# Kernel optimization log

Measured on AMD Instinct MI355X. Metric: run time of the kernel, lower is better.

## Reference

```python
import jax, jax.numpy as jnp
import numpy as np

B, C, H, W = 8, 512, 32, 32
MID = 64  # in_ch // k = 512 // 8
BN_EPS = 1e-5


def conv1x1(x, Wt, b):
    # x: [B,C,H,W], Wt: [O,C], b: [O]
    return jnp.einsum('bchw,oc->bohw', x, Wt) + b[None, :, None, None]


def batchnorm(x, gamma, beta):
    # train-mode BN: batch statistics over (B,H,W)
    mu = jnp.mean(x, axis=(0, 2, 3), keepdims=True)
    var = jnp.var(x, axis=(0, 2, 3), keepdims=True)
    xn = (x - mu) * jax.lax.rsqrt(var + BN_EPS)
    return xn * gamma[None, :, None, None] + beta[None, :, None, None]


def setup_inputs() -> dict:
    key = jax.random.key(0)
    ks = jax.random.split(key, 8)
    scale = 1.0 / np.sqrt(C)
    x = jax.random.normal(ks[0], (B, C, H, W), dtype=jnp.float32)
    Wf = jax.random.normal(ks[1], (MID, C), dtype=jnp.float32) * scale
    Wg = jax.random.normal(ks[2], (MID, C), dtype=jnp.float32) * scale
    Wh = jax.random.normal(ks[3], (MID, C), dtype=jnp.float32) * scale
    Wv = jax.random.normal(ks[4], (C, MID), dtype=jnp.float32) * (1.0 / np.sqrt(MID))
    return {
        'x': x,
        'Wf': Wf, 'bf': jnp.zeros((MID,), jnp.float32),
        'gamma_f': jnp.ones((MID,), jnp.float32), 'beta_f': jnp.zeros((MID,), jnp.float32),
        'Wg': Wg, 'bg': jnp.zeros((MID,), jnp.float32),
        'gamma_g': jnp.ones((MID,), jnp.float32), 'beta_g': jnp.zeros((MID,), jnp.float32),
        'Wh': Wh, 'bh': jnp.zeros((MID,), jnp.float32),
        'Wv': Wv, 'bv': jnp.zeros((C,), jnp.float32),
    }


def reference(x, Wf, bf, gamma_f, beta_f, Wg, bg, gamma_g, beta_g, Wh, bh, Wv, bv):
    b, c, h, w = x.shape
    hw = h * w
    f_x = jax.nn.relu(batchnorm(conv1x1(x, Wf, bf), gamma_f, beta_f)).reshape(b, MID, hw)
    g_x = jax.nn.relu(batchnorm(conv1x1(x, Wg, bg), gamma_g, beta_g)).reshape(b, MID, hw)
    h_x = conv1x1(x, Wh, bh).reshape(b, MID, hw)
    # z = f_x^T @ g_x : [B, HW, HW]
    z = jnp.einsum('bcn,bcm->bnm', f_x, g_x)
    # spectral normalization by the top singular value
    S = jnp.linalg.svd(z, compute_uv=False)  # sorted descending
    sigma = S[:, 0][:, None, None]
    attn = z / sigma
    # attn @ h_x^T -> [B, HW, MID], then permute to [B, MID, H, W]
    z2 = jnp.einsum('bnm,bcm->bcn', attn, h_x).reshape(b, MID, h, w)
    return conv1x1(z2, Wv, bv) + x
```

## Files before the change

kernel.cpp:

```cpp
#include <hip/hip_runtime.h>

#define B_   8
#define C_   512
#define HW_  1024
#define MID_ 64
#define NCOL (B_*HW_)
#define NROWS 192
#define EPS  1e-5f

#define YOFF  0
#define YSZ   (NROWS*NCOL)
#define SSOFF (YOFF+YSZ)
#define SSSZ  256
#define WOFF  (SSOFF+SSSZ)
#define WSZ   98304
#define CPOFF (WOFF+WSZ)

typedef unsigned short u16;
typedef __attribute__((ext_vector_type(8))) short short8;
typedef __attribute__((ext_vector_type(4))) float f32x4;

__device__ __forceinline__ u16 f2bf(float f) {
  unsigned u = __float_as_uint(f);
  unsigned r = u + 0x7fffu + ((u >> 16) & 1u);
  return (u16)(r >> 16);
}
__device__ __forceinline__ float bf2f(u16 h) {
  return __uint_as_float(((unsigned)h) << 16);
}
#define MFMA_B16(a,b,c) __builtin_amdgcn_mfma_f32_16x16x32_bf16(a,b,c,0,0,0)

__global__ __launch_bounds__(256) void k_prep(
    const float* __restrict__ Wf, const float* __restrict__ Wg,
    const float* __restrict__ Wh, float* __restrict__ ws)
{
  u16* Whi = (u16*)(ws + WOFF);
  u16* Wlo = Whi + NROWS*C_;
  const int e4 = blockIdx.x*256 + threadIdx.x;
  const int e  = e4*4;
  const int row = e >> 9, k = e & 511;
  const float* src = (row < 64) ? &Wf[row*C_ + k]
                   : (row < 128) ? &Wg[(row-64)*C_ + k]
                   : &Wh[(row-128)*C_ + k];
  const float4 v = *reinterpret_cast<const float4*>(src);
  u16 h0=f2bf(v.x), h1=f2bf(v.y), h2=f2bf(v.z), h3=f2bf(v.w);
  u16 l0=f2bf(v.x-bf2f(h0)), l1=f2bf(v.y-bf2f(h1)), l2=f2bf(v.z-bf2f(h2)), l3=f2bf(v.w-bf2f(h3));
  uint2 ph; ph.x = (unsigned)h0 | ((unsigned)h1<<16); ph.y = (unsigned)h2 | ((unsigned)h3<<16);
  uint2 pl; pl.x = (unsigned)l0 | ((unsigned)l1<<16); pl.y = (unsigned)l2 | ((unsigned)l3<<16);
  *reinterpret_cast<uint2*>(&Whi[e]) = ph;
  *reinterpret_cast<uint2*>(&Wlo[e]) = pl;
}

__global__ __launch_bounds__(256) void k_conv(
    const float* __restrict__ x,
    const float* __restrict__ bf, const float* __restrict__ bg, const float* __restrict__ bh,
    float* __restrict__ ws)
{
  __shared__ u16 Xh[8*32*8];
  __shared__ u16 Xl[8*32*8];
  const u16* Whi = (const u16*)(ws + WOFF);
  const u16* Wlo = Whi + NROWS*C_;
  const int n0  = blockIdx.x * 32;
  const int b   = n0 >> 10;
  const int hw0 = n0 & 1023;
  const int t   = threadIdx.x;
  const int lane = t & 63;
  const int wid  = t >> 6;
  const int wrow0 = wid * 48;
  const int cst  = t & 31;
  const int kg2  = t >> 5;
  const int lm   = lane & 15;
  const int lk   = lane >> 4;

  f32x4 acc[3][2];
  #pragma unroll
  for (int i=0;i<3;++i) { acc[i][0]=(f32x4)0.f; acc[i][1]=(f32x4)0.f; }

  for (int kk = 0; kk < C_; kk += 64) {
    __syncthreads();
    {
      const float* xp = x + ((size_t)(b*C_ + kk + kg2*8))*HW_ + hw0 + cst;
      u16 hb[8], lb[8];
      #pragma unroll
      for (int i=0;i<8;++i) {
        const float v = xp[(size_t)i*HW_];
        hb[i] = f2bf(v); lb[i] = f2bf(v - bf2f(hb[i]));
      }
      uint4 ph, pl;
      ph.x=(unsigned)hb[0]|((unsigned)hb[1]<<16); ph.y=(unsigned)hb[2]|((unsigned)hb[3]<<16);
      ph.z=(unsigned)hb[4]|((unsigned)hb[5]<<16); ph.w=(unsigned)hb[6]|((unsigned)hb[7]<<16);
      pl.x=(unsigned)lb[0]|((unsigned)lb[1]<<16); pl.y=(unsigned)lb[2]|((unsigned)lb[3]<<16);
      pl.z=(unsigned)lb[4]|((unsigned)lb[5]<<16); pl.w=(unsigned)lb[6]|((unsigned)lb[7]<<16);
      *reinterpret_cast<uint4*>(&Xh[(kg2*32+cst)*8]) = ph;
      *reinterpret_cast<uint4*>(&Xl[(kg2*32+cst)*8]) = pl;
    }
    __syncthreads();
    #pragma unroll
    for (int kb = 0; kb < 2; ++kb) {
      short8 bhf[2], blf[2];
      #pragma unroll
      for (int nt = 0; nt < 2; ++nt) {
        const int col = nt*16 + lm;
        const int idx = ((kb*4 + lk)*32 + col)*8;
        bhf[nt] = *reinterpret_cast<const short8*>(&Xh[idx]);
        blf[nt] = *reinterpret_cast<const short8*>(&Xl[idx]);
      }
      #pragma unroll
      for (int mt = 0; mt < 3; ++mt) {
        const int row = wrow0 + mt*16 + lm;
        const size_t widx = (size_t)row*C_ + kk + kb*32 + lk*8;
        const short8 ah = *reinterpret_cast<const short8*>(&Whi[widx]);
        const short8 al = *reinterpret_cast<const short8*>(&Wlo[widx]);
        #pragma unroll
        for (int nt = 0; nt < 2; ++nt) {
          acc[mt][nt] = MFMA_B16(ah, bhf[nt], acc[mt][nt]);
          acc[mt][nt] = MFMA_B16(al, bhf[nt], acc[mt][nt]);
          acc[mt][nt] = MFMA_B16(ah, blf[nt], acc[mt][nt]);
        }
      }
    }
  }
  #pragma unroll
  for (int mt = 0; mt < 3; ++mt) {
    const int rbase = wrow0 + mt*16;
    const float* bp = (rbase < 64) ? bf : (rbase < 128) ? bg : bh;
    const int rloc0 = (rbase & 63) + lk*4;
    #pragma unroll
    for (int nt = 0; nt < 2; ++nt) {
      const int col = n0 + nt*16 + lm;
      #pragma unroll
      for (int r = 0; r < 4; ++r) {
        const int row = rbase + lk*4 + r;
        ws[YOFF + (size_t)row*NCOL + col] = acc[mt][nt][r] + bp[rloc0 + r];
      }
    }
  }
}

__global__ __launch_bounds__(256) void k_stats(
    const float* __restrict__ gamma_f, const float* __restrict__ beta_f,
    const float* __restrict__ gamma_g, const float* __restrict__ beta_g,
    float* __restrict__ ws)
{
  const int r = blockIdx.x;
  const float4* Yr = reinterpret_cast<const float4*>(ws + YOFF + (size_t)r*NCOL);
  const int t = threadIdx.x;
  float s = 0.f, s2 = 0.f;
  for (int n = t; n < NCOL/4; n += 256) {
    const float4 v = Yr[n];
    s  += (v.x+v.y)+(v.z+v.w);
    s2 += (v.x*v.x+v.y*v.y)+(v.z*v.z+v.w*v.w);
  }
  __shared__ float sh[256], sh2[256];
  sh[t] = s; sh2[t] = s2;
  __syncthreads();
  for (int st = 128; st > 0; st >>= 1) {
    if (t < st) { sh[t] += sh[t+st]; sh2[t] += sh2[t+st]; }
    __syncthreads();
  }
  if (t == 0) {
    const float mean = sh[0] * (1.0f/NCOL);
    const float var  = sh2[0] * (1.0f/NCOL) - mean*mean;
    float g, be; int j;
    if (r < 64) { j = r;     g = gamma_f[j]; be = beta_f[j]; }
    else        { j = r-64;  g = gamma_g[j]; be = beta_g[j]; }
    const float sc = g * rsqrtf(var + EPS);
    const float sf = be - mean*sc;
    if (r < 64) { ws[SSOFF + j]       = sc; ws[SSOFF + 64  + j] = sf; }
    else        { ws[SSOFF + 128 + j] = sc; ws[SSOFF + 192 + j] = sf; }
  }
}

__global__ __launch_bounds__(256) void k_cpart(float* __restrict__ ws, int nchunk)
{
  __shared__ u16 Sh[3][64][72];
  __shared__ u16 Sl[3][64][72];
  const int chunk = blockIdx.x, b = blockIdx.y;
  const int chunkcols = 1024 / nchunk;
  const int bcol0 = b*1024 + chunk*chunkcols;
  const float* Y = ws + YOFF;
  const float* SS = ws + SSOFF;
  const int t = threadIdx.x;
  const int lane = t & 63, wid = t >> 6;
  const int lm = lane & 15, lk = lane >> 4;
  const int mt0 = (wid >> 1) * 2;
  const int nt0 = (wid & 1) * 2;

  f32x4 acc[3][2][2];
  #pragma unroll
  for (int p=0;p<3;++p) for (int i=0;i<2;++i) for (int j=0;j<2;++j) acc[p][i][j]=(f32x4)0.f;

  for (int kk = 0; kk < chunkcols; kk += 64) {
    __syncthreads();
    for (int q = t; q < 3072; q += 256) {
      const int mm = q >> 10, rem = q & 1023;
      const int r = rem >> 4, c4 = (rem & 15) * 4;
      const float4 v = *reinterpret_cast<const float4*>(
          &Y[(size_t)(mm*64 + r)*NCOL + bcol0 + kk + c4]);
      float v0, v1, v2, v3;
      if (mm < 2) {
        const float sc = SS[mm*128 + r], sf = SS[mm*128 + 64 + r];
        v0 = fmaxf(sc*v.x+sf, 0.f); v1 = fmaxf(sc*v.y+sf, 0.f);
        v2 = fmaxf(sc*v.z+sf, 0.f); v3 = fmaxf(sc*v.w+sf, 0.f);
      } else { v0=v.x; v1=v.y; v2=v.z; v3=v.w; }
      const u16 h0=f2bf(v0), h1=f2bf(v1), h2=f2bf(v2), h3=f2bf(v3);
      uint2 ph; ph.x=(unsigned)h0|((unsigned)h1<<16); ph.y=(unsigned)h2|((unsigned)h3<<16);
      uint2 pl;
      pl.x=(unsigned)f2bf(v0-bf2f(h0)) | ((unsigned)f2bf(v1-bf2f(h1))<<16);
      pl.y=(unsigned)f2bf(v2-bf2f(h2)) | ((unsigned)f2bf(v3-bf2f(h3))<<16);
      *reinterpret_cast<uint2*>(&Sh[mm][r][c4]) = ph;
      *reinterpret_cast<uint2*>(&Sl[mm][r][c4]) = pl;
    }
    __syncthreads();
    #pragma unroll
    for (int kb = 0; kb < 2; ++kb) {
      const int ko = kb*32 + lk*8;
      short8 ah[3][2], al[3][2];
      #pragma unroll
      for (int m = 0; m < 3; ++m)
        #pragma unroll
        for (int mi = 0; mi < 2; ++mi) {
          const int row = (mt0+mi)*16 + lm;
          ah[m][mi] = *reinterpret_cast<const short8*>(&Sh[m][row][ko]);
          al[m][mi] = *reinterpret_cast<const short8*>(&Sl[m][row][ko]);
        }
      short8 bhf[2][2], blf[2][2];
      #pragma unroll
      for (int m = 0; m < 2; ++m)
        #pragma unroll
        for (int ni = 0; ni < 2; ++ni) {
          const int row = (nt0+ni)*16 + lm;
          bhf[m][ni] = *reinterpret_cast<const short8*>(&Sh[m][row][ko]);
          blf[m][ni] = *reinterpret_cast<const short8*>(&Sl[m][row][ko]);
        }
      #pragma unroll
      for (int p = 0; p < 3; ++p) {
        const int am = p;
        const int bm = (p==0) ? 0 : 1;
        #pragma unroll
        for (int mi = 0; mi < 2; ++mi)
          #pragma unroll
          for (int ni = 0; ni < 2; ++ni) {
            acc[p][mi][ni] = MFMA_B16(ah[am][mi], bhf[bm][ni], acc[p][mi][ni]);
            acc[p][mi][ni] = MFMA_B16(al[am][mi], bhf[bm][ni], acc[p][mi][ni]);
            acc[p][mi][ni] = MFMA_B16(ah[am][mi], blf[bm][ni], acc[p][mi][ni]);
          }
      }
    }
  }
  float* cp = ws + CPOFF;
  #pragma unroll
  for (int p = 0; p < 3; ++p) {
    float* base = cp + ((size_t)((b*3+p)*nchunk + chunk))*4096;
    #pragma unroll
    for (int mi = 0; mi < 2; ++mi)
      #pragma unroll
      for (int ni = 0; ni < 2; ++ni) {
        const int col = (nt0+ni)*16 + lm;
        #pragma unroll
        for (int r = 0; r < 4; ++r) {
          const int row = (mt0+mi)*16 + lk*4 + r;
          base[(size_t)row*64 + col] = acc[p][mi][ni][r];
        }
      }
  }
}

__global__ __launch_bounds__(256) void k_creduce(float* __restrict__ ws, int nchunk)
{
  const int m = blockIdx.y;
  const int q = blockIdx.x*256 + threadIdx.x;
  const float4* src = reinterpret_cast<const float4*>(ws + CPOFF) + (size_t)m*nchunk*1024;
  const size_t cmoff = (size_t)CPOFF + (size_t)B_*3*nchunk*4096;
  float4 s = {0.f,0.f,0.f,0.f};
  for (int ch = 0; ch < nchunk; ++ch) {
    const float4 p = src[(size_t)ch*1024 + q];
    s.x+=p.x; s.y+=p.y; s.z+=p.z; s.w+=p.w;
  }
  *(reinterpret_cast<float4*>(ws + cmoff) + (size_t)m*1024 + q) = s;
}

__global__ __launch_bounds__(64) void k_sigma(float* __restrict__ ws, int nchunk)
{
  const int b = blockIdx.x;
  const int lane = threadIdx.x;
  const size_t cmoff = (size_t)CPOFF + (size_t)B_*3*nchunk*4096;
  const size_t isoff = cmoff + 24*4096;
  const float* Cf = ws + cmoff + (size_t)(b*3+0)*4096;
  const float* Cg = ws + cmoff + (size_t)(b*3+1)*4096;
  __shared__ float vsh[64];
  __shared__ float ush[64];
  float cfr[64], cgr[64];
  #pragma unroll
  for (int k4 = 0; k4 < 16; ++k4) {
    const float4 fa = *reinterpret_cast<const float4*>(&Cf[lane*64 + k4*4]);
    const float4 fc = *reinterpret_cast<const float4*>(&Cg[lane*64 + k4*4]);
    cfr[k4*4+0]=fa.x; cfr[k4*4+1]=fa.y; cfr[k4*4+2]=fa.z; cfr[k4*4+3]=fa.w;
    cgr[k4*4+0]=fc.x; cgr[k4*4+1]=fc.y; cgr[k4*4+2]=fc.z; cgr[k4*4+3]=fc.w;
  }
  float vloc = 0.125f;
  vsh[lane] = vloc;
  __syncthreads();
  float lambda = 0.f;
  #define NIT 20
  for (int it = 0; it <= NIT; ++it) {
    float u0=0.f,u1=0.f,u2=0.f,u3=0.f;
    #pragma unroll
    for (int j4 = 0; j4 < 16; ++j4) {
      const float4 vq = *reinterpret_cast<const float4*>(&vsh[j4*4]);
      u0 += cfr[j4*4+0]*vq.x; u1 += cfr[j4*4+1]*vq.y;
      u2 += cfr[j4*4+2]*vq.z; u3 += cfr[j4*4+3]*vq.w;
    }
    ush[lane] = (u0+u1)+(u2+u3);
    __syncthreads();
    float w0=0.f,w1=0.f,w2=0.f,w3=0.f;
    #pragma unroll
    for (int j4 = 0; j4 < 16; ++j4) {
      const float4 uq = *reinterpret_cast<const float4*>(&ush[j4*4]);
      w0 += cgr[j4*4+0]*uq.x; w1 += cgr[j4*4+1]*uq.y;
      w2 += cgr[j4*4+2]*uq.z; w3 += cgr[j4*4+3]*uq.w;
    }
    const float w = (w0+w1)+(w2+w3);
    if (it == NIT) {
      float num = vloc * w;
      #pragma unroll
      for (int off = 32; off > 0; off >>= 1) num += __shfl_xor(num, off);
      lambda = num;
    } else {
      float n2 = w*w;
      #pragma unroll
      for (int off = 32; off > 0; off >>= 1) n2 += __shfl_xor(n2, off);
      const float rn = rsqrtf(fmaxf(n2, 1e-30f));
      vloc = w * rn;
      vsh[lane] = vloc;
      __syncthreads();
    }
  }
  if (lane == 0) ws[isoff + b] = rsqrtf(fmaxf(lambda, 1e-30f));
}

__global__ __launch_bounds__(256) void k_ufold(const float* __restrict__ Wv,
                                               float* __restrict__ ws, int nchunk)
{
  __shared__ float Wt[64][64];
  __shared__ float Tl[64][64];
  const int rt = blockIdx.x, b = blockIdx.y;
  const size_t cmoff = (size_t)CPOFF + (size_t)B_*3*nchunk*4096;
  const size_t isoff = cmoff + 24*4096;
  const size_t uoff  = isoff + 16;
  const float* T = ws + cmoff + (size_t)(b*3+2)*4096;
  const float isig = ws[isoff + b];
  const int t = threadIdx.x;
  const int ti = t >> 4, tj = t & 15;
  for (int q = t; q < 1024; q += 256)
    *(reinterpret_cast<float4*>(&Tl[0][0]) + q) = *(reinterpret_cast<const float4*>(T) + q);
  for (int q = t; q < 1024; q += 256) {
    const int row = q >> 4;
    const int c4  = (q & 15) * 4;
    const float4 wv = *reinterpret_cast<const float4*>(&Wv[(size_t)(rt*64+row)*64 + c4]);
    Wt[c4+0][row]=wv.x; Wt[c4+1][row]=wv.y; Wt[c4+2][row]=wv.z; Wt[c4+3][row]=wv.w;
  }
  __syncthreads();
  float acc[4][4] = {};
  #pragma unroll
  for (int c = 0; c < 64; ++c) {
    const float4 a  = *reinterpret_cast<const float4*>(&Wt[c][ti*4]);
    const float4 bb = *reinterpret_cast<const float4*>(&Tl[c][tj*4]);
    acc[0][0]+=a.x*bb.x; acc[0][1]+=a.x*bb.y; acc[0][2]+=a.x*bb.z; acc[0][3]+=a.x*bb.w;
    acc[1][0]+=a.y*bb.x; acc[1][1]+=a.y*bb.y; acc[1][2]+=a.y*bb.z; acc[1][3]+=a.y*bb.w;
    acc[2][0]+=a.z*bb.x; acc[2][1]+=a.z*bb.y; acc[2][2]+=a.z*bb.z; acc[2][3]+=a.z*bb.w;
    acc[3][0]+=a.w*bb.x; acc[3][1]+=a.w*bb.y; acc[3][2]+=a.w*bb.z; acc[3][3]+=a.w*bb.w;
  }
  #pragma unroll
  for (int i = 0; i < 4; ++i) {
    float4 o; o.x = acc[i][0]*isig; o.y = acc[i][1]*isig; o.z = acc[i][2]*isig; o.w = acc[i][3]*isig;
    *reinterpret_cast<float4*>(&ws[uoff + ((size_t)b*512 + rt*64 + ti*4+i)*64 + tj*4]) = o;
  }
}

__global__ __launch_bounds__(256) void k_final(
    const float* __restrict__ x, const float* __restrict__ bv,
    float* __restrict__ out, const float* __restrict__ ws, int nchunk)
{
  __shared__ float Ut[64][64];
  __shared__ float Fl[64][64];
  const int nt = blockIdx.x, ot = blockIdx.y, b = blockIdx.z;
  const size_t uoff = (size_t)CPOFF + (size_t)B_*3*nchunk*4096 + 24*4096 + 16;
  const float* scF = ws + SSOFF; const float* sfF = ws + SSOFF + 64;
  const int t = threadIdx.x;
  const int ti = t >> 4, tj = t & 15;
  for (int q = t; q < 1024; q += 256) {
    const int row = q >> 4;
    const int k4  = (q & 15) * 4;
    const float4 uv = *reinterpret_cast<const float4*>(
        &ws[uoff + ((size_t)b*512 + ot*64 + row)*64 + k4]);
    Ut[k4+0][row]=uv.x; Ut[k4+1][row]=uv.y; Ut[k4+2][row]=uv.z; Ut[k4+3][row]=uv.w;
  }
  for (int q = t; q < 1024; q += 256) {
    const int k  = q >> 4;
    const int c4 = (q & 15) * 4;
    const float4 yv = *reinterpret_cast<const float4*>(
        &ws[YOFF + (size_t)k*NCOL + b*1024 + nt*64 + c4]);
    const float s = scF[k], f = sfF[k];
    Fl[k][c4+0]=fmaxf(s*yv.x+f,0.f); Fl[k][c4+1]=fmaxf(s*yv.y+f,0.f);
    Fl[k][c4+2]=fmaxf(s*yv.z+f,0.f); Fl[k][c4+3]=fmaxf(s*yv.w+f,0.f);
  }
  __syncthreads();
  float acc[4][4] = {};
  #pragma unroll
  for (int k = 0; k < 64; ++k) {
    const float4 a  = *reinterpret_cast<const float4*>(&Ut[k][ti*4]);
    const float4 bb = *reinterpret_cast<const float4*>(&Fl[k][tj*4]);
    acc[0][0]+=a.x*bb.x; acc[0][1]+=a.x*bb.y; acc[0][2]+=a.x*bb.z; acc[0][3]+=a.x*bb.w;
    acc[1][0]+=a.y*bb.x; acc[1][1]+=a.y*bb.y; acc[1][2]+=a.y*bb.z; acc[1][3]+=a.y*bb.w;
    acc[2][0]+=a.z*bb.x; acc[2][1]+=a.z*bb.y; acc[2][2]+=a.z*bb.z; acc[2][3]+=a.z*bb.w;
    acc[3][0]+=a.w*bb.x; acc[3][1]+=a.w*bb.y; acc[3][2]+=a.w*bb.z; acc[3][3]+=a.w*bb.w;
  }
  #pragma unroll
  for (int i = 0; i < 4; ++i) {
    const int oc = ot*64 + ti*4 + i;
    const float bvv = bv[oc];
    const size_t base = ((size_t)b*C_ + oc)*HW_ + nt*64 + tj*4;
    const float4 xv = *reinterpret_cast<const float4*>(&x[base]);
    float4 o;
    o.x = acc[i][0]+bvv+xv.x; o.y = acc[i][1]+bvv+xv.y;
    o.z = acc[i][2]+bvv+xv.z; o.w = acc[i][3]+bvv+xv.w;
    *reinterpret_cast<float4*>(&out[base]) = o;
  }
}

extern "C" void kernel_launch(void* const* d_in, const int* in_sizes, int n_in,
                              void* d_out, int out_size, void* d_ws, size_t ws_size,
                              hipStream_t stream) {
  (void)in_sizes; (void)n_in; (void)out_size;
  const float* x       = (const float*)d_in[0];
  const float* Wf      = (const float*)d_in[1];
  const float* bf      = (const float*)d_in[2];
  const float* gamma_f = (const float*)d_in[3];
  const float* beta_f  = (const float*)d_in[4];
  const float* Wg      = (const float*)d_in[5];
  const float* bg      = (const float*)d_in[6];
  const float* gamma_g = (const float*)d_in[7];
  const float* beta_g  = (const float*)d_in[8];
  const float* Wh      = (const float*)d_in[9];
  const float* bh      = (const float*)d_in[10];
  const float* Wv      = (const float*)d_in[11];
  const float* bv      = (const float*)d_in[12];
  float* out = (float*)d_out;
  float* ws  = (float*)d_ws;

  auto need = [](int nc) -> size_t {
    return ((size_t)CPOFF + (size_t)B_*3*nc*4096 + 24*4096 + 16 + (size_t)B_*512*64) * 4;
  };
  const int nchunk = (ws_size >= need(16)) ? 16 : (ws_size >= need(8)) ? 8 : 4;

  k_prep   <<<96,             256, 0, stream>>>(Wf, Wg, Wh, ws);
  k_conv   <<<256,            256, 0, stream>>>(x, bf, bg, bh, ws);
  k_stats  <<<128,            256, 0, stream>>>(gamma_f, beta_f, gamma_g, beta_g, ws);
  k_cpart  <<<dim3(nchunk,8), 256, 0, stream>>>(ws, nchunk);
  k_creduce<<<dim3(4,24),     256, 0, stream>>>(ws, nchunk);
  k_sigma  <<<8,               64, 0, stream>>>(ws, nchunk);
  k_ufold  <<<dim3(8,8),      256, 0, stream>>>(Wv, ws, nchunk);
  k_final  <<<dim3(16,8,8),   256, 0, stream>>>(x, bv, out, ws, nchunk);
}
```

Measured before the change: 92.85 us.

## Fuse all stages into one persistent kernel with atomic grid barriers

Replaces the eight separate kernel launches with a single persistent 256-block kernel that runs each stage in turn and separates them with a software grid barrier built on an atomic counter. Shared memory is overlaid through a union, and the work split is changed per stage (stats split across two blocks per row, cpart with 32 fixed chunks, final handling four column tiles per block). This removes launch overhead and inter-kernel gaps between many small stages. In exchange it relies on all 256 blocks being co-resident for the spin barrier, and each barrier adds its own latency.

```diff
diff --git a/kernel.cpp b/kernel.cpp
--- a/kernel.cpp
+++ b/kernel.cpp
@@ -3,18 +3,26 @@
 #define B_   8
 #define C_   512
 #define HW_  1024
-#define MID_ 64
 #define NCOL (B_*HW_)
 #define NROWS 192
 #define EPS  1e-5f
-
-#define YOFF  0
-#define YSZ   (NROWS*NCOL)
-#define SSOFF (YOFF+YSZ)
-#define SSSZ  256
-#define WOFF  (SSOFF+SSSZ)
-#define WSZ   98304
-#define CPOFF (WOFF+WSZ)
+#define NBLK 256
+#define NCHUNK 32
+
+#define YOFF   0
+#define YSZ    (NROWS*NCOL)
+#define WOFF   (YOFF+YSZ)
+#define WSZ    98304
+#define SPOFF  (WOFF+WSZ)
+#define SPSZ   512
+#define CTROFF (SPOFF+SPSZ)
+#define CTRSZ  16
+#define CP2OFF (CTROFF+CTRSZ)
+#define CP2SZ  (B_*3*NCHUNK*4096)
+#define CMOFF  (CP2OFF+CP2SZ)
+#define CMSZ   (24*4096)
+#define ISOFF  (CMOFF+CMSZ)
+#define UOFF   (ISOFF+16)
 
 typedef unsigned short u16;
 typedef __attribute__((ext_vector_type(8))) short short8;
@@ -30,176 +38,193 @@
 }
 #define MFMA_B16(a,b,c) __builtin_amdgcn_mfma_f32_16x16x32_bf16(a,b,c,0,0,0)
 
-__global__ __launch_bounds__(256) void k_prep(
-    const float* __restrict__ Wf, const float* __restrict__ Wg,
-    const float* __restrict__ Wh, float* __restrict__ ws)
+#define FMA16(a, bb) \
+  acc[0][0]+=a.x*bb.x; acc[0][1]+=a.x*bb.y; acc[0][2]+=a.x*bb.z; acc[0][3]+=a.x*bb.w; \
+  acc[1][0]+=a.y*bb.x; acc[1][1]+=a.y*bb.y; acc[1][2]+=a.y*bb.z; acc[1][3]+=a.y*bb.w; \
+  acc[2][0]+=a.z*bb.x; acc[2][1]+=a.z*bb.y; acc[2][2]+=a.z*bb.z; acc[2][3]+=a.z*bb.w; \
+  acc[3][0]+=a.w*bb.x; acc[3][1]+=a.w*bb.y; acc[3][2]+=a.w*bb.z; acc[3][3]+=a.w*bb.w;
+
+union alignas(16) SMem {
+  struct { u16 Xh[8*32*8]; u16 Xl[8*32*8]; } conv;
+  struct { u16 Sh[3][64][40]; u16 Sl[3][64][40]; float sc[128]; float sf[128]; } cpart;
+  struct { float sh[256]; float sh2[256]; } stats;
+  struct { float v[64]; float u[64]; } sigma;
+  struct { float Tl[64][64]; } ufold;
+  struct { float Ut[64][64]; float Fl[64][64]; float scF[64]; float sfF[64]; } fin;
+};
+
+__device__ __forceinline__ void gbar(unsigned* ctr, unsigned phase) {
+  __syncthreads();
+  if (threadIdx.x == 0) {
+    __hip_atomic_fetch_add(ctr, 1u, __ATOMIC_ACQ_REL, __HIP_MEMORY_SCOPE_AGENT);
+    const unsigned tgt = (unsigned)NBLK * (phase + 1u);
+    while (__hip_atomic_load(ctr, __ATOMIC_ACQUIRE, __HIP_MEMORY_SCOPE_AGENT) < tgt)
+      __builtin_amdgcn_s_sleep(4);
+  }
+  __syncthreads();
+  __builtin_amdgcn_fence(__ATOMIC_ACQUIRE, "agent");
+}
+
+__global__ void k_init(float* __restrict__ ws) {
+  if (threadIdx.x == 0) *reinterpret_cast<unsigned*>(ws + CTROFF) = 0u;
+}
+
+__global__ __launch_bounds__(256, 2) void k_mega(
+    const float* __restrict__ x,
+    const float* __restrict__ Wf, const float* __restrict__ bf,
+    const float* __restrict__ gamma_f, const float* __restrict__ beta_f,
+    const float* __restrict__ Wg, const float* __restrict__ bg,
+    const float* __restrict__ gamma_g, const float* __restrict__ beta_g,
+    const float* __restrict__ Wh, const float* __restrict__ bh,
+    const float* __restrict__ Wv, const float* __restrict__ bv,
+    float* __restrict__ out, float* __restrict__ ws)
 {
+  __shared__ SMem sm;
+  const int bid = blockIdx.x;
+  const int t = threadIdx.x;
+  unsigned* ctr = reinterpret_cast<unsigned*>(ws + CTROFF);
   u16* Whi = (u16*)(ws + WOFF);
   u16* Wlo = Whi + NROWS*C_;
-  const int e4 = blockIdx.x*256 + threadIdx.x;
-  const int e  = e4*4;
-  const int row = e >> 9, k = e & 511;
-  const float* src = (row < 64) ? &Wf[row*C_ + k]
-                   : (row < 128) ? &Wg[(row-64)*C_ + k]
-                   : &Wh[(row-128)*C_ + k];
-  const float4 v = *reinterpret_cast<const float4*>(src);
-  u16 h0=f2bf(v.x), h1=f2bf(v.y), h2=f2bf(v.z), h3=f2bf(v.w);
-  u16 l0=f2bf(v.x-bf2f(h0)), l1=f2bf(v.y-bf2f(h1)), l2=f2bf(v.z-bf2f(h2)), l3=f2bf(v.w-bf2f(h3));
-  uint2 ph; ph.x = (unsigned)h0 | ((unsigned)h1<<16); ph.y = (unsigned)h2 | ((unsigned)h3<<16);
-  uint2 pl; pl.x = (unsigned)l0 | ((unsigned)l1<<16); pl.y = (unsigned)l2 | ((unsigned)l3<<16);
-  *reinterpret_cast<uint2*>(&Whi[e]) = ph;
-  *reinterpret_cast<uint2*>(&Wlo[e]) = pl;
-}
-
-__global__ __launch_bounds__(256) void k_conv(
-    const float* __restrict__ x,
-    const float* __restrict__ bf, const float* __restrict__ bg, const float* __restrict__ bh,
-    float* __restrict__ ws)
-{
-  __shared__ u16 Xh[8*32*8];
-  __shared__ u16 Xl[8*32*8];
-  const u16* Whi = (const u16*)(ws + WOFF);
-  const u16* Wlo = Whi + NROWS*C_;
-  const int n0  = blockIdx.x * 32;
-  const int b   = n0 >> 10;
-  const int hw0 = n0 & 1023;
-  const int t   = threadIdx.x;
-  const int lane = t & 63;
-  const int wid  = t >> 6;
-  const int wrow0 = wid * 48;
-  const int cst  = t & 31;
-  const int kg2  = t >> 5;
-  const int lm   = lane & 15;
-  const int lk   = lane >> 4;
-
-  f32x4 acc[3][2];
-  #pragma unroll
-  for (int i=0;i<3;++i) { acc[i][0]=(f32x4)0.f; acc[i][1]=(f32x4)0.f; }
-
-  for (int kk = 0; kk < C_; kk += 64) {
+
+  {
+    const int e4 = bid*256 + t;
+    if (e4 < NROWS*C_/4) {
+      const int e = e4*4;
+      const int row = e >> 9, k = e & 511;
+      const float* src = (row < 64) ? &Wf[row*C_ + k]
+                       : (row < 128) ? &Wg[(row-64)*C_ + k]
+                       : &Wh[(row-128)*C_ + k];
+      const float4 v = *reinterpret_cast<const float4*>(src);
+      u16 h0=f2bf(v.x), h1=f2bf(v.y), h2=f2bf(v.z), h3=f2bf(v.w);
+      u16 l0=f2bf(v.x-bf2f(h0)), l1=f2bf(v.y-bf2f(h1)), l2=f2bf(v.z-bf2f(h2)), l3=f2bf(v.w-bf2f(h3));
+      uint2 ph; ph.x = (unsigned)h0 | ((unsigned)h1<<16); ph.y = (unsigned)h2 | ((unsigned)h3<<16);
+      uint2 pl; pl.x = (unsigned)l0 | ((unsigned)l1<<16); pl.y = (unsigned)l2 | ((unsigned)l3<<16);
+      *reinterpret_cast<uint2*>(&Whi[e]) = ph;
+      *reinterpret_cast<uint2*>(&Wlo[e]) = pl;
+    }
+  }
+  gbar(ctr, 0);
+
+  {
+    const int n0  = bid * 32;
+    const int b   = n0 >> 10;
+    const int hw0 = n0 & 1023;
+    const int lane = t & 63, wid = t >> 6;
+    const int wrow0 = wid * 48;
+    const int cst = t & 31, kg2 = t >> 5;
+    const int lm = lane & 15, lk = lane >> 4;
+
+    f32x4 acc[3][2];
+    #pragma unroll
+    for (int i=0;i<3;++i) { acc[i][0]=(f32x4)0.f; acc[i][1]=(f32x4)0.f; }
+
+    for (int kk = 0; kk < C_; kk += 64) {
+      __syncthreads();
+      {
+        const float* xp = x + ((size_t)(b*C_ + kk + kg2*8))*HW_ + hw0 + cst;
+        u16 hb[8], lb[8];
+        #pragma unroll
+        for (int i=0;i<8;++i) {
+          const float v = xp[(size_t)i*HW_];
+          hb[i] = f2bf(v); lb[i] = f2bf(v - bf2f(hb[i]));
+        }
+        uint4 ph, pl;
+        ph.x=(unsigned)hb[0]|((unsigned)hb[1]<<16); ph.y=(unsigned)hb[2]|((unsigned)hb[3]<<16);
+        ph.z=(unsigned)hb[4]|((unsigned)hb[5]<<16); ph.w=(unsigned)hb[6]|((unsigned)hb[7]<<16);
+        pl.x=(unsigned)lb[0]|((unsigned)lb[1]<<16); pl.y=(unsigned)lb[2]|((unsigned)lb[3]<<16);
+        pl.z=(unsigned)lb[4]|((unsigned)lb[5]<<16); pl.w=(unsigned)lb[6]|((unsigned)lb[7]<<16);
+        *reinterpret_cast<uint4*>(&sm.conv.Xh[(kg2*32+cst)*8]) = ph;
+        *reinterpret_cast<uint4*>(&sm.conv.Xl[(kg2*32+cst)*8]) = pl;
+      }
+      __syncthreads();
+      #pragma unroll
+      for (int kb = 0; kb < 2; ++kb) {
+        short8 bhf[2], blf[2];
+        #pragma unroll
+        for (int nt = 0; nt < 2; ++nt) {
+          const int col = nt*16 + lm;
+          const int idx = ((kb*4 + lk)*32 + col)*8;
+          bhf[nt] = *reinterpret_cast<const short8*>(&sm.conv.Xh[idx]);
+          blf[nt] = *reinterpret_cast<const short8*>(&sm.conv.Xl[idx]);
+        }
+        #pragma unroll
+        for (int mt = 0; mt < 3; ++mt) {
+          const int row = wrow0 + mt*16 + lm;
+          const size_t widx = (size_t)row*C_ + kk + kb*32 + lk*8;
+          const short8 ah = *reinterpret_cast<const short8*>(&Whi[widx]);
+          const short8 al = *reinterpret_cast<const short8*>(&Wlo[widx]);
+          #pragma unroll
+          for (int nt = 0; nt < 2; ++nt) {
+            acc[mt][nt] = MFMA_B16(ah, bhf[nt], acc[mt][nt]);
+            acc[mt][nt] = MFMA_B16(al, bhf[nt], acc[mt][nt]);
+            acc[mt][nt] = MFMA_B16(ah, blf[nt], acc[mt][nt]);
+          }
+        }
+      }
+    }
+    #pragma unroll
+    for (int mt = 0; mt < 3; ++mt) {
+      const int rbase = wrow0 + mt*16;
+      const float* bp = (rbase < 64) ? bf : (rbase < 128) ? bg : bh;
+      const int rloc0 = (rbase & 63) + lk*4;
+      #pragma unroll
+      for (int nt = 0; nt < 2; ++nt) {
+        const int col = n0 + nt*16 + lm;
+        #pragma unroll
+        for (int r = 0; r < 4; ++r) {
+          const int row = rbase + lk*4 + r;
+          ws[YOFF + (size_t)row*NCOL + col] = acc[mt][nt][r] + bp[rloc0 + r];
+        }
+      }
+    }
+  }
+  gbar(ctr, 1);
+
+  {
+    const int row = bid >> 1, half = bid & 1;
+    const float4* Yr = reinterpret_cast<const float4*>(ws + YOFF + (size_t)row*NCOL + half*4096);
+    float s = 0.f, s2 = 0.f;
+    for (int q = t; q < 1024; q += 256) {
+      const float4 v = Yr[q];
+      s  += (v.x+v.y)+(v.z+v.w);
+      s2 += (v.x*v.x+v.y*v.y)+(v.z*v.z+v.w*v.w);
+    }
+    sm.stats.sh[t] = s; sm.stats.sh2[t] = s2;
     __syncthreads();
-    {
-      const float* xp = x + ((size_t)(b*C_ + kk + kg2*8))*HW_ + hw0 + cst;
-      u16 hb[8], lb[8];
-      #pragma unroll
-      for (int i=0;i<8;++i) {
-        const float v = xp[(size_t)i*HW_];
-        hb[i] = f2bf(v); lb[i] = f2bf(v - bf2f(hb[i]));
-      }
-      uint4 ph, pl;
-      ph.x=(unsigned)hb[0]|((unsigned)hb[1]<<16); ph.y=(unsigned)hb[2]|((unsigned)hb[3]<<16);
-      ph.z=(unsigned)hb[4]|((unsigned)hb[5]<<16); ph.w=(unsigned)hb[6]|((unsigned)hb[7]<<16);
-      pl.x=(unsigned)lb[0]|((unsigned)lb[1]<<16); pl.y=(unsigned)lb[2]|((unsigned)lb[3]<<16);
-      pl.z=(unsigned)lb[4]|((unsigned)lb[5]<<16); pl.w=(unsigned)lb[6]|((unsigned)lb[7]<<16);
-      *reinterpret_cast<uint4*>(&Xh[(kg2*32+cst)*8]) = ph;
-      *reinterpret_cast<uint4*>(&Xl[(kg2*32+cst)*8]) = pl;
+    for (int st = 128; st > 0; st >>= 1) {
+      if (t < st) { sm.stats.sh[t] += sm.stats.sh[t+st]; sm.stats.sh2[t] += sm.stats.sh2[t+st]; }
+      __syncthreads();
+    }
+    if (t == 0) {
+      ws[SPOFF + row*4 + half*2 + 0] = sm.stats.sh[0];
+      ws[SPOFF + row*4 + half*2 + 1] = sm.stats.sh2[0];
+    }
+  }
+  gbar(ctr, 2);
+
+  {
+    const int chunk = bid & 31, b = bid >> 5;
+    if (t < 128) {
+      const float* sp = ws + SPOFF;
+      const float s  = sp[t*4+0] + sp[t*4+2];
+      const float s2 = sp[t*4+1] + sp[t*4+3];
+      const float mean = s*(1.0f/NCOL);
+      const float var  = s2*(1.0f/NCOL) - mean*mean;
+      const float g  = (t < 64) ? gamma_f[t] : gamma_g[t-64];
+      const float be = (t < 64) ? beta_f[t]  : beta_g[t-64];
+      const float sc = g * rsqrtf(var + EPS);
+      sm.cpart.sc[t] = sc; sm.cpart.sf[t] = be - mean*sc;
     }
     __syncthreads();
-    #pragma unroll
-    for (int kb = 0; kb < 2; ++kb) {
-      short8 bhf[2], blf[2];
-      #pragma unroll
-      for (int nt = 0; nt < 2; ++nt) {
-        const int col = nt*16 + lm;
-        const int idx = ((kb*4 + lk)*32 + col)*8;
-        bhf[nt] = *reinterpret_cast<const short8*>(&Xh[idx]);
-        blf[nt] = *reinterpret_cast<const short8*>(&Xl[idx]);
-      }
-      #pragma unroll
-      for (int mt = 0; mt < 3; ++mt) {
-        const int row = wrow0 + mt*16 + lm;
-        const size_t widx = (size_t)row*C_ + kk + kb*32 + lk*8;
-        const short8 ah = *reinterpret_cast<const short8*>(&Whi[widx]);
-        const short8 al = *reinterpret_cast<const short8*>(&Wlo[widx]);
-        #pragma unroll
-        for (int nt = 0; nt < 2; ++nt) {
-          acc[mt][nt] = MFMA_B16(ah, bhf[nt], acc[mt][nt]);
-          acc[mt][nt] = MFMA_B16(al, bhf[nt], acc[mt][nt]);
-          acc[mt][nt] = MFMA_B16(ah, blf[nt], acc[mt][nt]);
-        }
-      }
-    }
-  }
-  #pragma unroll
-  for (int mt = 0; mt < 3; ++mt) {
-    const int rbase = wrow0 + mt*16;
-    const float* bp = (rbase < 64) ? bf : (rbase < 128) ? bg : bh;
-    const int rloc0 = (rbase & 63) + lk*4;
-    #pragma unroll
-    for (int nt = 0; nt < 2; ++nt) {
-      const int col = n0 + nt*16 + lm;
-      #pragma unroll
-      for (int r = 0; r < 4; ++r) {
-        const int row = rbase + lk*4 + r;
-        ws[YOFF + (size_t)row*NCOL + col] = acc[mt][nt][r] + bp[rloc0 + r];
-      }
-    }
-  }
-}
-
-__global__ __launch_bounds__(256) void k_stats(
-    const float* __restrict__ gamma_f, const float* __restrict__ beta_f,
-    const float* __restrict__ gamma_g, const float* __restrict__ beta_g,
-    float* __restrict__ ws)
-{
-  const int r = blockIdx.x;
-  const float4* Yr = reinterpret_cast<const float4*>(ws + YOFF + (size_t)r*NCOL);
-  const int t = threadIdx.x;
-  float s = 0.f, s2 = 0.f;
-  for (int n = t; n < NCOL/4; n += 256) {
-    const float4 v = Yr[n];
-    s  += (v.x+v.y)+(v.z+v.w);
-    s2 += (v.x*v.x+v.y*v.y)+(v.z*v.z+v.w*v.w);
-  }
-  __shared__ float sh[256], sh2[256];
-  sh[t] = s; sh2[t] = s2;
-  __syncthreads();
-  for (int st = 128; st > 0; st >>= 1) {
-    if (t < st) { sh[t] += sh[t+st]; sh2[t] += sh2[t+st]; }
-    __syncthreads();
-  }
-  if (t == 0) {
-    const float mean = sh[0] * (1.0f/NCOL);
-    const float var  = sh2[0] * (1.0f/NCOL) - mean*mean;
-    float g, be; int j;
-    if (r < 64) { j = r;     g = gamma_f[j]; be = beta_f[j]; }
-    else        { j = r-64;  g = gamma_g[j]; be = beta_g[j]; }
-    const float sc = g * rsqrtf(var + EPS);
-    const float sf = be - mean*sc;
-    if (r < 64) { ws[SSOFF + j]       = sc; ws[SSOFF + 64  + j] = sf; }
-    else        { ws[SSOFF + 128 + j] = sc; ws[SSOFF + 192 + j] = sf; }
-  }
-}
-
-__global__ __launch_bounds__(256) void k_cpart(float* __restrict__ ws, int nchunk)
-{
-  __shared__ u16 Sh[3][64][72];
-  __shared__ u16 Sl[3][64][72];
-  const int chunk = blockIdx.x, b = blockIdx.y;
-  const int chunkcols = 1024 / nchunk;
-  const int bcol0 = b*1024 + chunk*chunkcols;
-  const float* Y = ws + YOFF;
-  const float* SS = ws + SSOFF;
-  const int t = threadIdx.x;
-  const int lane = t & 63, wid = t >> 6;
-  const int lm = lane & 15, lk = lane >> 4;
-  const int mt0 = (wid >> 1) * 2;
-  const int nt0 = (wid & 1) * 2;
-
-  f32x4 acc[3][2][2];
-  #pragma unroll
-  for (int p=0;p<3;++p) for (int i=0;i<2;++i) for (int j=0;j<2;++j) acc[p][i][j]=(f32x4)0.f;
-
-  for (int kk = 0; kk < chunkcols; kk += 64) {
-    __syncthreads();
-    for (int q = t; q < 3072; q += 256) {
-      const int mm = q >> 10, rem = q & 1023;
-      const int r = rem >> 4, c4 = (rem & 15) * 4;
+    const int bcol0 = b*1024 + chunk*32;
+    for (int q = t; q < 1536; q += 256) {
+      const int mm = q >> 9, rem = q & 511;
+      const int r = rem >> 3, c4 = (rem & 7) * 4;
       const float4 v = *reinterpret_cast<const float4*>(
-          &Y[(size_t)(mm*64 + r)*NCOL + bcol0 + kk + c4]);
+          &ws[YOFF + (size_t)(mm*64 + r)*NCOL + bcol0 + c4]);
       float v0, v1, v2, v3;
       if (mm < 2) {
-        const float sc = SS[mm*128 + r], sf = SS[mm*128 + 64 + r];
+        const float sc = sm.cpart.sc[mm*64 + r], sf = sm.cpart.sf[mm*64 + r];
         v0 = fmaxf(sc*v.x+sf, 0.f); v1 = fmaxf(sc*v.y+sf, 0.f);
         v2 = fmaxf(sc*v.z+sf, 0.f); v3 = fmaxf(sc*v.w+sf, 0.f);
       } else { v0=v.x; v1=v.y; v2=v.z; v3=v.w; }
@@ -208,21 +233,23 @@
       uint2 pl;
       pl.x=(unsigned)f2bf(v0-bf2f(h0)) | ((unsigned)f2bf(v1-bf2f(h1))<<16);
       pl.y=(unsigned)f2bf(v2-bf2f(h2)) | ((unsigned)f2bf(v3-bf2f(h3))<<16);
-      *reinterpret_cast<uint2*>(&Sh[mm][r][c4]) = ph;
-      *reinterpret_cast<uint2*>(&Sl[mm][r][c4]) = pl;
+      *reinterpret_cast<uint2*>(&sm.cpart.Sh[mm][r][c4]) = ph;
+      *reinterpret_cast<uint2*>(&sm.cpart.Sl[mm][r][c4]) = pl;
     }
     __syncthreads();
-    #pragma unroll
-    for (int kb = 0; kb < 2; ++kb) {
-      const int ko = kb*32 + lk*8;
+    {
+      const int lane = t & 63, wid = t >> 6;
+      const int lm = lane & 15, lk = lane >> 4;
+      const int mt0 = (wid >> 1)*2, nt0 = (wid & 1)*2;
+      const int ko = lk*8;
       short8 ah[3][2], al[3][2];
       #pragma unroll
       for (int m = 0; m < 3; ++m)
         #pragma unroll
         for (int mi = 0; mi < 2; ++mi) {
           const int row = (mt0+mi)*16 + lm;
-          ah[m][mi] = *reinterpret_cast<const short8*>(&Sh[m][row][ko]);
-          al[m][mi] = *reinterpret_cast<const short8*>(&Sl[m][row][ko]);
+          ah[m][mi] = *reinterpret_cast<const short8*>(&sm.cpart.Sh[m][row][ko]);
+          al[m][mi] = *reinterpret_cast<const short8*>(&sm.cpart.Sl[m][row][ko]);
         }
       short8 bhf[2][2], blf[2][2];
       #pragma unroll
@@ -230,9 +257,12 @@
         #pragma unroll
         for (int ni = 0; ni < 2; ++ni) {
           const int row = (nt0+ni)*16 + lm;
-          bhf[m][ni] = *reinterpret_cast<const short8*>(&Sh[m][row][ko]);
-          blf[m][ni] = *reinterpret_cast<const short8*>(&Sl[m][row][ko]);
-        }
+          bhf[m][ni] = *reinterpret_cast<const short8*>(&sm.cpart.Sh[m][row][ko]);
+          blf[m][ni] = *reinterpret_cast<const short8*>(&sm.cpart.Sl[m][row][ko]);
+        }
+      f32x4 acc2[3][2][2];
+      #pragma unroll
+      for (int p=0;p<3;++p) for (int i=0;i<2;++i) for (int j=0;j<2;++j) acc2[p][i][j]=(f32x4)0.f;
       #pragma unroll
       for (int p = 0; p < 3; ++p) {
         const int am = p;
@@ -241,198 +271,189 @@
         for (int mi = 0; mi < 2; ++mi)
           #pragma unroll
           for (int ni = 0; ni < 2; ++ni) {
-            acc[p][mi][ni] = MFMA_B16(ah[am][mi], bhf[bm][ni], acc[p][mi][ni]);
-            acc[p][mi][ni] = MFMA_B16(al[am][mi], bhf[bm][ni], acc[p][mi][ni]);
-            acc[p][mi][ni] = MFMA_B16(ah[am][mi], blf[bm][ni], acc[p][mi][ni]);
+            acc2[p][mi][ni] = MFMA_B16(ah[am][mi], bhf[bm][ni], acc2[p][mi][ni]);
+            acc2[p][mi][ni] = MFMA_B16(al[am][mi], bhf[bm][ni], acc2[p][mi][ni]);
+            acc2[p][mi][ni] = MFMA_B16(ah[am][mi], blf[bm][ni], acc2[p][mi][ni]);
           }
       }
-    }
-  }
-  float* cp = ws + CPOFF;
-  #pragma unroll
-  for (int p = 0; p < 3; ++p) {
-    float* base = cp + ((size_t)((b*3+p)*nchunk + chunk))*4096;
+      float* cp = ws + CP2OFF;
+      #pragma unroll
+      for (int p = 0; p < 3; ++p) {
+        float* base = cp + ((size_t)((b*3+p)*NCHUNK + chunk))*4096;
+        #pragma unroll
+        for (int mi = 0; mi < 2; ++mi)
+          #pragma unroll
+          for (int ni = 0; ni < 2; ++ni) {
+            const int col = (nt0+ni)*16 + lm;
+            #pragma unroll
+            for (int r = 0; r < 4; ++r) {
+              const int row = (mt0+mi)*16 + lk*4 + r;
+              base[(size_t)row*64 + col] = acc2[p][mi][ni][r];
+            }
+          }
+      }
+    }
+  }
+  gbar(ctr, 3);
+
+  {
+    const float* cp2 = ws + CP2OFF;
+    float* cm = ws + CMOFF;
+    for (unsigned idx = (unsigned)bid*256 + t; idx < 24u*4096u; idx += 65536u) {
+      const unsigned m = idx >> 12, e = idx & 4095u;
+      const float* s = cp2 + (size_t)m*NCHUNK*4096 + e;
+      float a = 0.f;
+      #pragma unroll
+      for (int ch = 0; ch < NCHUNK; ++ch) a += s[(size_t)ch*4096];
+      cm[(size_t)m*4096 + e] = a;
+    }
+  }
+  gbar(ctr, 4);
+
+  if (bid < 8) {
+    const int b = bid;
+    const int lane = t;
+    const float* Cf = ws + CMOFF + (size_t)(b*3+0)*4096;
+    const float* Cg = ws + CMOFF + (size_t)(b*3+1)*4096;
+    float cfr[64], cgr[64];
+    if (t < 64) {
+      #pragma unroll
+      for (int k4 = 0; k4 < 16; ++k4) {
+        const float4 fa = *reinterpret_cast<const float4*>(&Cf[lane*64 + k4*4]);
+        const float4 fc = *reinterpret_cast<const float4*>(&Cg[lane*64 + k4*4]);
+        cfr[k4*4+0]=fa.x; cfr[k4*4+1]=fa.y; cfr[k4*4+2]=fa.z; cfr[k4*4+3]=fa.w;
+        cgr[k4*4+0]=fc.x; cgr[k4*4+1]=fc.y; cgr[k4*4+2]=fc.z; cgr[k4*4+3]=fc.w;
+      }
+    }
+    float vloc = 0.125f;
+    if (t < 64) sm.sigma.v[lane] = vloc;
+    __syncthreads();
+    const int NIT = 14;
+    float lambda = 0.f;
+    for (int it = 0; it <= NIT; ++it) {
+      float w = 0.f;
+      if (t < 64) {
+        float u0=0.f,u1=0.f,u2=0.f,u3=0.f;
+        #pragma unroll
+        for (int j4 = 0; j4 < 16; ++j4) {
+          const float4 vq = *reinterpret_cast<const float4*>(&sm.sigma.v[j4*4]);
+          u0 += cfr[j4*4+0]*vq.x; u1 += cfr[j4*4+1]*vq.y;
+          u2 += cfr[j4*4+2]*vq.z; u3 += cfr[j4*4+3]*vq.w;
+        }
+        sm.sigma.u[lane] = (u0+u1)+(u2+u3);
+      }
+      __syncthreads();
+      if (t < 64) {
+        float w0=0.f,w1=0.f,w2=0.f,w3=0.f;
+        #pragma unroll
+        for (int j4 = 0; j4 < 16; ++j4) {
+          const float4 uq = *reinterpret_cast<const float4*>(&sm.sigma.u[j4*4]);
+          w0 += cgr[j4*4+0]*uq.x; w1 += cgr[j4*4+1]*uq.y;
+          w2 += cgr[j4*4+2]*uq.z; w3 += cgr[j4*4+3]*uq.w;
+        }
+        w = (w0+w1)+(w2+w3);
+      }
+      if (it == NIT) {
+        if (t < 64) {
+          float num = vloc * w;
+          #pragma unroll
+          for (int off = 32; off > 0; off >>= 1) num += __shfl_xor(num, off);
+          lambda = num;
+        }
+      } else {
+        if (t < 64) {
+          float n2 = w*w;
+          #pragma unroll
+          for (int off = 32; off > 0; off >>= 1) n2 += __shfl_xor(n2, off);
+          const float rn = rsqrtf(fmaxf(n2, 1e-30f));
+          vloc = w * rn;
+        }
+        __syncthreads();
+        if (t < 64) sm.sigma.v[lane] = vloc;
+        __syncthreads();
+      }
+    }
+    if (t == 0) ws[ISOFF + b] = rsqrtf(fmaxf(lambda, 1e-30f));
+  }
+  gbar(ctr, 5);
+
+  {
+    const int b = bid >> 5, rt = bid & 31;
+    const float* T = ws + CMOFF + (size_t)(b*3+2)*4096;
+    for (int q = t; q < 1024; q += 256)
+      *(reinterpret_cast<float4*>(&sm.ufold.Tl[0][0]) + q) = *(reinterpret_cast<const float4*>(T) + q);
+    __syncthreads();
+    const float isig = ws[ISOFF + b];
+    const int row = rt*16 + (t >> 4), col0 = (t & 15)*4;
+    float ax=0.f, ay=0.f, az=0.f, aw=0.f;
     #pragma unroll
-    for (int mi = 0; mi < 2; ++mi)
-      #pragma unroll
-      for (int ni = 0; ni < 2; ++ni) {
-        const int col = (nt0+ni)*16 + lm;
-        #pragma unroll
-        for (int r = 0; r < 4; ++r) {
-          const int row = (mt0+mi)*16 + lk*4 + r;
-          base[(size_t)row*64 + col] = acc[p][mi][ni][r];
-        }
-      }
-  }
-}
-
-__global__ __launch_bounds__(256) void k_creduce(float* __restrict__ ws, int nchunk)
-{
-  const int m = blockIdx.y;
-  const int q = blockIdx.x*256 + threadIdx.x;
-  const float4* src = reinterpret_cast<const float4*>(ws + CPOFF) + (size_t)m*nchunk*1024;
-  const size_t cmoff = (size_t)CPOFF + (size_t)B_*3*nchunk*4096;
-  float4 s = {0.f,0.f,0.f,0.f};
-  for (int ch = 0; ch < nchunk; ++ch) {
-    const float4 p = src[(size_t)ch*1024 + q];
-    s.x+=p.x; s.y+=p.y; s.z+=p.z; s.w+=p.w;
-  }
-  *(reinterpret_cast<float4*>(ws + cmoff) + (size_t)m*1024 + q) = s;
-}
-
-__global__ __launch_bounds__(64) void k_sigma(float* __restrict__ ws, int nchunk)
-{
-  const int b = blockIdx.x;
-  const int lane = threadIdx.x;
-  const size_t cmoff = (size_t)CPOFF + (size_t)B_*3*nchunk*4096;
-  const size_t isoff = cmoff + 24*4096;
-  const float* Cf = ws + cmoff + (size_t)(b*3+0)*4096;
-  const float* Cg = ws + cmoff + (size_t)(b*3+1)*4096;
-  __shared__ float vsh[64];
-  __shared__ float ush[64];
-  float cfr[64], cgr[64];
-  #pragma unroll
-  for (int k4 = 0; k4 < 16; ++k4) {
-    const float4 fa = *reinterpret_cast<const float4*>(&Cf[lane*64 + k4*4]);
-    const float4 fc = *reinterpret_cast<const float4*>(&Cg[lane*64 + k4*4]);
-    cfr[k4*4+0]=fa.x; cfr[k4*4+1]=fa.y; cfr[k4*4+2]=fa.z; cfr[k4*4+3]=fa.w;
-    cgr[k4*4+0]=fc.x; cgr[k4*4+1]=fc.y; cgr[k4*4+2]=fc.z; cgr[k4*4+3]=fc.w;
-  }
-  float vloc = 0.125f;
-  vsh[lane] = vloc;
-  __syncthreads();
-  float lambda = 0.f;
-  #define NIT 20
-  for (int it = 0; it <= NIT; ++it) {
-    float u0=0.f,u1=0.f,u2=0.f,u3=0.f;
-    #pragma unroll
-    for (int j4 = 0; j4 < 16; ++j4) {
-      const float4 vq = *reinterpret_cast<const float4*>(&vsh[j4*4]);
-      u0 += cfr[j4*4+0]*vq.x; u1 += cfr[j4*4+1]*vq.y;
-      u2 += cfr[j4*4+2]*vq.z; u3 += cfr[j4*4+3]*vq.w;
-    }
-    ush[lane] = (u0+u1)+(u2+u3);
-    __syncthreads();
-    float w0=0.f,w1=0.f,w2=0.f,w3=0.f;
-    #pragma unroll
-    for (int j4 = 0; j4 < 16; ++j4) {
-      const float4 uq = *reinterpret_cast<const float4*>(&ush[j4*4]);
-      w0 += cgr[j4*4+0]*uq.x; w1 += cgr[j4*4+1]*uq.y;
-      w2 += cgr[j4*4+2]*uq.z; w3 += cgr[j4*4+3]*uq.w;
-    }
-    const float w = (w0+w1)+(w2+w3);
-    if (it == NIT) {
-      float num = vloc * w;
-      #pragma unroll
-      for (int off = 32; off > 0; off >>= 1) num += __shfl_xor(num, off);
-      lambda = num;
-    } else {
-      float n2 = w*w;
-      #pragma unroll
-      for (int off = 32; off > 0; off >>= 1) n2 += __shfl_xor(n2, off);
-      const float rn = rsqrtf(fmaxf(n2, 1e-30f));
-      vloc = w * rn;
-      vsh[lane] = vloc;
-      __syncthreads();
-    }
-  }
-  if (lane == 0) ws[isoff + b] = rsqrtf(fmaxf(lambda, 1e-30f));
-}
-
-__global__ __launch_bounds__(256) void k_ufold(const float* __restrict__ Wv,
-                                               float* __restrict__ ws, int nchunk)
-{
-  __shared__ float Wt[64][64];
-  __shared__ float Tl[64][64];
-  const int rt = blockIdx.x, b = blockIdx.y;
-  const size_t cmoff = (size_t)CPOFF + (size_t)B_*3*nchunk*4096;
-  const size_t isoff = cmoff + 24*4096;
-  const size_t uoff  = isoff + 16;
-  const float* T = ws + cmoff + (size_t)(b*3+2)*4096;
-  const float isig = ws[isoff + b];
-  const int t = threadIdx.x;
-  const int ti = t >> 4, tj = t & 15;
-  for (int q = t; q < 1024; q += 256)
-    *(reinterpret_cast<float4*>(&Tl[0][0]) + q) = *(reinterpret_cast<const float4*>(T) + q);
-  for (int q = t; q < 1024; q += 256) {
-    const int row = q >> 4;
-    const int c4  = (q & 15) * 4;
-    const float4 wv = *reinterpret_cast<const float4*>(&Wv[(size_t)(rt*64+row)*64 + c4]);
-    Wt[c4+0][row]=wv.x; Wt[c4+1][row]=wv.y; Wt[c4+2][row]=wv.z; Wt[c4+3][row]=wv.w;
-  }
-  __syncthreads();
-  float acc[4][4] = {};
-  #pragma unroll
-  for (int c = 0; c < 64; ++c) {
-    const float4 a  = *reinterpret_cast<const float4*>(&Wt[c][ti*4]);
-    const float4 bb = *reinterpret_cast<const float4*>(&Tl[c][tj*4]);
-    acc[0][0]+=a.x*bb.x; acc[0][1]+=a.x*bb.y; acc[0][2]+=a.x*bb.z; acc[0][3]+=a.x*bb.w;
-    acc[1][0]+=a.y*bb.x; acc[1][1]+=a.y*bb.y; acc[1][2]+=a.y*bb.z; acc[1][3]+=a.y*bb.w;
-    acc[2][0]+=a.z*bb.x; acc[2][1]+=a.z*bb.y; acc[2][2]+=a.z*bb.z; acc[2][3]+=a.z*bb.w;
-    acc[3][0]+=a.w*bb.x; acc[3][1]+=a.w*bb.y; acc[3][2]+=a.w*bb.z; acc[3][3]+=a.w*bb.w;
-  }
-  #pragma unroll
-  for (int i = 0; i < 4; ++i) {
-    float4 o; o.x = acc[i][0]*isig; o.y = acc[i][1]*isig; o.z = acc[i][2]*isig; o.w = acc[i][3]*isig;
-    *reinterpret_cast<float4*>(&ws[uoff + ((size_t)b*512 + rt*64 + ti*4+i)*64 + tj*4]) = o;
-  }
-}
-
-__global__ __launch_bounds__(256) void k_final(
-    const float* __restrict__ x, const float* __restrict__ bv,
-    float* __restrict__ out, const float* __restrict__ ws, int nchunk)
-{
-  __shared__ float Ut[64][64];
-  __shared__ float Fl[64][64];
-  const int nt = blockIdx.x, ot = blockIdx.y, b = blockIdx.z;
-  const size_t uoff = (size_t)CPOFF + (size_t)B_*3*nchunk*4096 + 24*4096 + 16;
-  const float* scF = ws + SSOFF; const float* sfF = ws + SSOFF + 64;
-  const int t = threadIdx.x;
-  const int ti = t >> 4, tj = t & 15;
-  for (int q = t; q < 1024; q += 256) {
-    const int row = q >> 4;
-    const int k4  = (q & 15) * 4;
-    const float4 uv = *reinterpret_cast<const float4*>(
-        &ws[uoff + ((size_t)b*512 + ot*64 + row)*64 + k4]);
-    Ut[k4+0][row]=uv.x; Ut[k4+1][row]=uv.y; Ut[k4+2][row]=uv.z; Ut[k4+3][row]=uv.w;
-  }
-  for (int q = t; q < 1024; q += 256) {
-    const int k  = q >> 4;
-    const int c4 = (q & 15) * 4;
-    const float4 yv = *reinterpret_cast<const float4*>(
-        &ws[YOFF + (size_t)k*NCOL + b*1024 + nt*64 + c4]);
-    const float s = scF[k], f = sfF[k];
-    Fl[k][c4+0]=fmaxf(s*yv.x+f,0.f); Fl[k][c4+1]=fmaxf(s*yv.y+f,0.f);
-    Fl[k][c4+2]=fmaxf(s*yv.z+f,0.f); Fl[k][c4+3]=fmaxf(s*yv.w+f,0.f);
-  }
-  __syncthreads();
-  float acc[4][4] = {};
-  #pragma unroll
-  for (int k = 0; k < 64; ++k) {
-    const float4 a  = *reinterpret_cast<const float4*>(&Ut[k][ti*4]);
-    const float4 bb = *reinterpret_cast<const float4*>(&Fl[k][tj*4]);
-    acc[0][0]+=a.x*bb.x; acc[0][1]+=a.x*bb.y; acc[0][2]+=a.x*bb.z; acc[0][3]+=a.x*bb.w;
-    acc[1][0]+=a.y*bb.x; acc[1][1]+=a.y*bb.y; acc[1][2]+=a.y*bb.z; acc[1][3]+=a.y*bb.w;
-    acc[2][0]+=a.z*bb.x; acc[2][1]+=a.z*bb.y; acc[2][2]+=a.z*bb.z; acc[2][3]+=a.z*bb.w;
-    acc[3][0]+=a.w*bb.x; acc[3][1]+=a.w*bb.y; acc[3][2]+=a.w*bb.z; acc[3][3]+=a.w*bb.w;
-  }
-  #pragma unroll
-  for (int i = 0; i < 4; ++i) {
-    const int oc = ot*64 + ti*4 + i;
-    const float bvv = bv[oc];
-    const size_t base = ((size_t)b*C_ + oc)*HW_ + nt*64 + tj*4;
-    const float4 xv = *reinterpret_cast<const float4*>(&x[base]);
-    float4 o;
-    o.x = acc[i][0]+bvv+xv.x; o.y = acc[i][1]+bvv+xv.y;
-    o.z = acc[i][2]+bvv+xv.z; o.w = acc[i][3]+bvv+xv.w;
-    *reinterpret_cast<float4*>(&out[base]) = o;
+    for (int c = 0; c < 64; ++c) {
+      const float wv = Wv[(size_t)row*64 + c];
+      const float4 tv = *reinterpret_cast<const float4*>(&sm.ufold.Tl[c][col0]);
+      ax += wv*tv.x; ay += wv*tv.y; az += wv*tv.z; aw += wv*tv.w;
+    }
+    float4 o; o.x = ax*isig; o.y = ay*isig; o.z = az*isig; o.w = aw*isig;
+    *reinterpret_cast<float4*>(&ws[UOFF + ((size_t)b*512 + row)*64 + col0]) = o;
+  }
+  gbar(ctr, 6);
+
+  {
+    const int b = bid >> 5, ot = (bid >> 2) & 7, ntg = bid & 3;
+    if (t < 64) {
+      const float* sp = ws + SPOFF;
+      const float s  = sp[t*4+0] + sp[t*4+2];
+      const float s2 = sp[t*4+1] + sp[t*4+3];
+      const float mean = s*(1.0f/NCOL);
+      const float var  = s2*(1.0f/NCOL) - mean*mean;
+      const float sc = gamma_f[t] * rsqrtf(var + EPS);
+      sm.fin.scF[t] = sc; sm.fin.sfF[t] = beta_f[t] - mean*sc;
+    }
+    for (int q = t; q < 1024; q += 256) {
+      const int row = q >> 4, k4 = (q & 15)*4;
+      const float4 uv = *reinterpret_cast<const float4*>(
+          &ws[UOFF + ((size_t)b*512 + ot*64 + row)*64 + k4]);
+      sm.fin.Ut[k4+0][row]=uv.x; sm.fin.Ut[k4+1][row]=uv.y;
+      sm.fin.Ut[k4+2][row]=uv.z; sm.fin.Ut[k4+3][row]=uv.w;
+    }
+    const int ti = t >> 4, tj = t & 15;
+    for (int nt = 0; nt < 4; ++nt) {
+      __syncthreads();
+      const int ncol = ntg*4 + nt;
+      for (int q = t; q < 1024; q += 256) {
+        const int k = q >> 4, c4 = (q & 15)*4;
+        const float4 yv = *reinterpret_cast<const float4*>(
+            &ws[YOFF + (size_t)k*NCOL + b*1024 + ncol*64 + c4]);
+        const float s = sm.fin.scF[k], f = sm.fin.sfF[k];
+        sm.fin.Fl[k][c4+0]=fmaxf(s*yv.x+f,0.f); sm.fin.Fl[k][c4+1]=fmaxf(s*yv.y+f,0.f);
+        sm.fin.Fl[k][c4+2]=fmaxf(s*yv.z+f,0.f); sm.fin.Fl[k][c4+3]=fmaxf(s*yv.w+f,0.f);
+      }
+      __syncthreads();
+      float acc[4][4] = {};
+      #pragma unroll
+      for (int k = 0; k < 64; ++k) {
+        const float4 a  = *reinterpret_cast<const float4*>(&sm.fin.Ut[k][ti*4]);
+        const float4 bb = *reinterpret_cast<const float4*>(&sm.fin.Fl[k][tj*4]);
+        FMA16(a, bb)
+      }
+      #pragma unroll
+      for (int i = 0; i < 4; ++i) {
+        const int oc = ot*64 + ti*4 + i;
+        const float bvv = bv[oc];
+        const size_t base = ((size_t)b*C_ + oc)*HW_ + ncol*64 + tj*4;
+        const float4 xv = *reinterpret_cast<const float4*>(&x[base]);
+        float4 o;
+        o.x = acc[i][0]+bvv+xv.x; o.y = acc[i][1]+bvv+xv.y;
+        o.z = acc[i][2]+bvv+xv.z; o.w = acc[i][3]+bvv+xv.w;
+        *reinterpret_cast<float4*>(&out[base]) = o;
+      }
+    }
   }
 }
 
 extern "C" void kernel_launch(void* const* d_in, const int* in_sizes, int n_in,
                               void* d_out, int out_size, void* d_ws, size_t ws_size,
                               hipStream_t stream) {
-  (void)in_sizes; (void)n_in; (void)out_size;
+  (void)in_sizes; (void)n_in; (void)out_size; (void)ws_size;
   const float* x       = (const float*)d_in[0];
   const float* Wf      = (const float*)d_in[1];
   const float* bf      = (const float*)d_in[2];
@@ -449,17 +470,8 @@
   float* out = (float*)d_out;
   float* ws  = (float*)d_ws;
 
-  auto need = [](int nc) -> size_t {
-    return ((size_t)CPOFF + (size_t)B_*3*nc*4096 + 24*4096 + 16 + (size_t)B_*512*64) * 4;
-  };
-  const int nchunk = (ws_size >= need(16)) ? 16 : (ws_size >= need(8)) ? 8 : 4;
-
-  k_prep   <<<96,             256, 0, stream>>>(Wf, Wg, Wh, ws);
-  k_conv   <<<256,            256, 0, stream>>>(x, bf, bg, bh, ws);
-  k_stats  <<<128,            256, 0, stream>>>(gamma_f, beta_f, gamma_g, beta_g, ws);
-  k_cpart  <<<dim3(nchunk,8), 256, 0, stream>>>(ws, nchunk);
-  k_creduce<<<dim3(4,24),     256, 0, stream>>>(ws, nchunk);
-  k_sigma  <<<8,               64, 0, stream>>>(ws, nchunk);
-  k_ufold  <<<dim3(8,8),      256, 0, stream>>>(Wv, ws, nchunk);
-  k_final  <<<dim3(16,8,8),   256, 0, stream>>>(x, bv, out, ws, nchunk);
-}
+  k_init<<<1, 64, 0, stream>>>(ws);
+  k_mega<<<NBLK, 256, 0, stream>>>(x, Wf, bf, gamma_f, beta_f,
+                                   Wg, bg, gamma_g, beta_g,
+                                   Wh, bh, Wv, bv, out, ws);
+}
```

After: 252.0 us. 171% more time.
